# Kernel tuning notes

Measured on AMD Instinct MI355X. Metric: run time of the kernel, lower is better.

Reference implementation:

```python
import jax, jax.numpy as jnp
import numpy as np

N_NODES = 100000
N_EDGES = 1600000
D_FEAT = 64
UNITS = [128, 128]


def setup_inputs() -> dict:
    key = jax.random.key(0)
    ks = jax.random.split(key, 8)
    row = jax.random.randint(ks[0], (N_EDGES,), 0, N_NODES, dtype=jnp.int32)
    col = jax.random.randint(ks[1], (N_EDGES,), 0, N_NODES, dtype=jnp.int32)
    vals = jax.random.uniform(ks[2], (N_EDGES,), dtype=jnp.float32)
    H = jax.random.normal(ks[3], (N_NODES, D_FEAT), dtype=jnp.float32)
    W1 = jax.random.normal(ks[4], (D_FEAT, UNITS[0]), dtype=jnp.float32) * (1.0 / np.sqrt(D_FEAT))
    b1 = jnp.zeros((UNITS[0],), dtype=jnp.float32)
    W2 = jax.random.normal(ks[5], (UNITS[0], UNITS[1]), dtype=jnp.float32) * (1.0 / np.sqrt(UNITS[0]))
    b2 = jnp.zeros((UNITS[1],), dtype=jnp.float32)
    return {"row": row, "col": col, "vals": vals, "H": H,
            "W1": W1, "b1": b1, "W2": W2, "b2": b2}


def _spmm(row, col, vals, H, n_nodes):
    # sparse A (COO) @ dense H: gather source rows, scale, scatter-add to dest
    return jax.ops.segment_sum(vals[:, None] * H[col], row, num_segments=n_nodes)


def reference(row, col, vals, H, W1, b1, W2, b2):
    n = H.shape[0]
    # layer 0: AH @ W1 + b1, relu (source bug: relu applied since i < num_units-1)
    AH = _spmm(row, col, vals, H, n)
    H1 = jax.nn.relu(AH @ W1 + b1)
    # layer 1: same structure, also relu per source's activation condition
    AH1 = _spmm(row, col, vals, H1, n)
    H2 = jax.nn.relu(AH1 @ W2 + b2)
    return H2
```

## Files before the change

### kernel.cpp

```cpp
#include <hip/hip_runtime.h>


#define NFEAT 64
#define NHID 128
#define BSHIFT 9
#define BROWS (1 << BSHIFT)
#define NB_MAX 256

typedef __attribute__((ext_vector_type(8))) short bf16x8;
typedef __attribute__((ext_vector_type(4))) float f32x4;
typedef __attribute__((ext_vector_type(2))) float f32x2;

__device__ __forceinline__ unsigned short f2bf(float x) {
  unsigned u = __float_as_uint(x);
  unsigned r = (u + 0x7FFFu + ((u >> 16) & 1u)) >> 16;
  return (unsigned short)r;
}
__device__ __forceinline__ unsigned pack2(float a, float b) {
  return (unsigned)f2bf(a) | ((unsigned)f2bf(b) << 16);
}

__device__ __forceinline__ unsigned pk_fp8x4(float a, float b, float c, float d) {
  int w = __builtin_amdgcn_cvt_pk_fp8_f32(a, b, 0, false);
  w = __builtin_amdgcn_cvt_pk_fp8_f32(c, d, w, true);
  return (unsigned)w;
}
__device__ __forceinline__ unsigned char f2fp8(float x) {
  return (unsigned char)(__builtin_amdgcn_cvt_pk_fp8_f32(x, 0.f, 0, false) & 0xFF);
}

__device__ __forceinline__ void acc16(f32x2* a, uint4 q, float v) {
  f32x2 vv = {v, v};
  a[0] += vv * __builtin_amdgcn_cvt_pk_f32_fp8(q.x, false);
  a[1] += vv * __builtin_amdgcn_cvt_pk_f32_fp8(q.x, true);
  a[2] += vv * __builtin_amdgcn_cvt_pk_f32_fp8(q.y, false);
  a[3] += vv * __builtin_amdgcn_cvt_pk_f32_fp8(q.y, true);
  a[4] += vv * __builtin_amdgcn_cvt_pk_f32_fp8(q.z, false);
  a[5] += vv * __builtin_amdgcn_cvt_pk_f32_fp8(q.z, true);
  a[6] += vv * __builtin_amdgcn_cvt_pk_f32_fp8(q.w, false);
  a[7] += vv * __builtin_amdgcn_cvt_pk_f32_fp8(q.w, true);
}

template <int RS>
__device__ __forceinline__ void gather_row(
    const int2* __restrict__ sedge, const uint4* __restrict__ Hq,
    int beg, int end, int f, f32x2* a) {
  int j = beg;
  if ((j & 1) && j < end) {
    int2 ev = sedge[j];
    acc16(a, Hq[ev.x * RS + f], __int_as_float(ev.y));
    ++j;
  }
  if (j + 4 <= end) {
    const int4* mp = (const int4*)sedge;
    int4 m0 = mp[j >> 1], m1 = mp[(j >> 1) + 1];
    while (j + 8 <= end) {
      uint4 q0 = Hq[m0.x * RS + f];
      uint4 q1 = Hq[m0.z * RS + f];
      uint4 q2 = Hq[m1.x * RS + f];
      uint4 q3 = Hq[m1.z * RS + f];
      int4 n0 = mp[(j >> 1) + 2];
      int4 n1 = mp[(j >> 1) + 3];
      acc16(a, q0, __int_as_float(m0.y));
      acc16(a, q1, __int_as_float(m0.w));
      acc16(a, q2, __int_as_float(m1.y));
      acc16(a, q3, __int_as_float(m1.w));
      m0 = n0;
      m1 = n1;
      j += 4;
    }
    uint4 q0 = Hq[m0.x * RS + f];
    uint4 q1 = Hq[m0.z * RS + f];
    uint4 q2 = Hq[m1.x * RS + f];
    uint4 q3 = Hq[m1.z * RS + f];
    acc16(a, q0, __int_as_float(m0.y));
    acc16(a, q1, __int_as_float(m0.w));
    acc16(a, q2, __int_as_float(m1.y));
    acc16(a, q3, __int_as_float(m1.w));
    j += 4;
  }
  for (; j < end; ++j) {
    int2 ev = sedge[j];
    acc16(a, Hq[ev.x * RS + f], __int_as_float(ev.y));
  }
}

__global__ __launch_bounds__(256) void prep_kernel(
    const float* __restrict__ H, const float* __restrict__ W1,
    const float* __restrict__ W2, unsigned char* __restrict__ Hf8,
    unsigned short* __restrict__ Wsw1, unsigned short* __restrict__ Wsw2,
    int n8) {
  const int total = n8 + 64 * 128 + 128 * 128;
  for (int w = blockIdx.x * 256 + threadIdx.x; w < total; w += gridDim.x * 256) {
    if (w < n8) {
      float4 a = ((const float4*)H)[2 * w];
      float4 b = ((const float4*)H)[2 * w + 1];
      ((uint2*)Hf8)[w] = make_uint2(pk_fp8x4(a.x, a.y, a.z, a.w),
                                    pk_fp8x4(b.x, b.y, b.z, b.w));
    } else {
      int idx = w - n8;
      const float* W = W1;
      unsigned short* Wsw = Wsw1;
      if (idx >= 64 * 128) {
        idx -= 64 * 128;
        W = W2;
        Wsw = Wsw2;
      }
      int j = idx & 7, q = (idx >> 3) & 3, nn = (idx >> 5) & 127, kt = idx >> 12;
      int k = kt * 32 + q * 8 + j;
      Wsw[idx] = f2bf(W[(size_t)k * 128 + nn]);
    }
  }
}

__global__ __launch_bounds__(256) void bhist_kernel(
    const int* __restrict__ row, int* __restrict__ bcnt, int n_edges, int nb) {
  __shared__ int h[NB_MAX];
  for (int i = threadIdx.x; i < NB_MAX; i += 256) h[i] = 0;
  __syncthreads();
  const int n4 = n_edges >> 2;
  for (int i = blockIdx.x * 256 + threadIdx.x; i < n4; i += gridDim.x * 256) {
    int4 r4 = ((const int4*)row)[i];
    atomicAdd(&h[r4.x >> BSHIFT], 1);
    atomicAdd(&h[r4.y >> BSHIFT], 1);
    atomicAdd(&h[r4.z >> BSHIFT], 1);
    atomicAdd(&h[r4.w >> BSHIFT], 1);
  }
  if (blockIdx.x == 0 && threadIdx.x < (n_edges & 3))
    atomicAdd(&h[row[(n4 << 2) + threadIdx.x] >> BSHIFT], 1);
  __syncthreads();
  for (int i = threadIdx.x; i < nb; i += 256)
    if (h[i]) atomicAdd(&bcnt[i], h[i]);
}

__global__ __launch_bounds__(NB_MAX) void bscan_kernel(
    const int* __restrict__ bcnt, int* __restrict__ bbase, int* __restrict__ cur,
    int* __restrict__ row_ptr, int nb, int n) {
  __shared__ int sm[NB_MAX];
  int t = threadIdx.x;
  int v = (t < nb) ? bcnt[t] : 0;
  sm[t] = v;
  __syncthreads();
  for (int off = 1; off < NB_MAX; off <<= 1) {
    int u = (t >= off) ? sm[t - off] : 0;
    __syncthreads();
    sm[t] += u;
    __syncthreads();
  }
  if (t < nb) {
    bbase[t] = sm[t] - v;
    cur[t] = sm[t] - v;
  }
  if (t == nb - 1) {
    bbase[nb] = sm[t];
    row_ptr[n] = sm[t];
  }
}

__global__ __launch_bounds__(1024) void partition_kernel(
    const int* __restrict__ row, const int* __restrict__ col,
    const float* __restrict__ vals, int* __restrict__ cur,
    int2* __restrict__ bedge, int n_edges) {
  __shared__ int h[NB_MAX], base[NB_MAX], rk[NB_MAX];
  for (int i = threadIdx.x; i < NB_MAX; i += 1024) {
    h[i] = 0;
    rk[i] = 0;
  }
  __syncthreads();
  const int t0 = blockIdx.x * 1024 + threadIdx.x;
  const int T = gridDim.x * 1024;
  const int n4 = n_edges >> 2;
  for (int i = t0; i < n4; i += T) {
    int4 r4 = ((const int4*)row)[i];
    atomicAdd(&h[r4.x >> BSHIFT], 1);
    atomicAdd(&h[r4.y >> BSHIFT], 1);
    atomicAdd(&h[r4.z >> BSHIFT], 1);
    atomicAdd(&h[r4.w >> BSHIFT], 1);
  }
  if (blockIdx.x == 0 && threadIdx.x < (n_edges & 3))
    atomicAdd(&h[row[(n4 << 2) + threadIdx.x] >> BSHIFT], 1);
  __syncthreads();
  for (int i = threadIdx.x; i < NB_MAX; i += 1024)
    base[i] = h[i] ? atomicAdd(&cur[i], h[i]) : 0;
  __syncthreads();
  for (int i = t0; i < n4; i += T) {
    int4 r4 = ((const int4*)row)[i];
    int4 c4 = ((const int4*)col)[i];
    float4 v4 = ((const float4*)vals)[i];
    {
      int b = r4.x >> BSHIFT;
      int p = base[b] + atomicAdd(&rk[b], 1);
      bedge[p] = make_int2(((r4.x & (BROWS - 1)) << 17) | c4.x, __float_as_int(v4.x));
    }
    {
      int b = r4.y >> BSHIFT;
      int p = base[b] + atomicAdd(&rk[b], 1);
      bedge[p] = make_int2(((r4.y & (BROWS - 1)) << 17) | c4.y, __float_as_int(v4.y));
    }
    {
      int b = r4.z >> BSHIFT;
      int p = base[b] + atomicAdd(&rk[b], 1);
      bedge[p] = make_int2(((r4.z & (BROWS - 1)) << 17) | c4.z, __float_as_int(v4.z));
    }
    {
      int b = r4.w >> BSHIFT;
      int p = base[b] + atomicAdd(&rk[b], 1);
      bedge[p] = make_int2(((r4.w & (BROWS - 1)) << 17) | c4.w, __float_as_int(v4.w));
    }
  }
  if (blockIdx.x == 0 && threadIdx.x < (n_edges & 3)) {
    int e = (n4 << 2) + threadIdx.x;
    int r = row[e];
    int b = r >> BSHIFT;
    int p = base[b] + atomicAdd(&rk[b], 1);
    bedge[p] = make_int2(((r & (BROWS - 1)) << 17) | col[e], __float_as_int(vals[e]));
  }
}

__global__ __launch_bounds__(1024) void bucket_csr_kernel(
    const int* __restrict__ bbase, const int2* __restrict__ bedge,
    int* __restrict__ row_ptr, int2* __restrict__ sedge, int n) {
  __shared__ int cnt[BROWS];
  __shared__ int sm[BROWS];
  const int b = blockIdx.x;
  const int t = threadIdx.x;
  const int beg = bbase[b], end = bbase[b + 1];
  if (t < BROWS) cnt[t] = 0;
  __syncthreads();
  for (int j = beg + t; j < end; j += 1024)
    atomicAdd(&cnt[((unsigned)bedge[j].x) >> 17], 1);
  __syncthreads();
  int v = (t < BROWS) ? cnt[t] : 0;
  if (t < BROWS) sm[t] = v;
  __syncthreads();
  for (int off = 1; off < BROWS; off <<= 1) {
    int u = (t >= off && t < BROWS) ? sm[t - off] : 0;
    __syncthreads();
    if (t < BROWS) sm[t] += u;
    __syncthreads();
  }
  int incl = (t < BROWS) ? sm[t] : 0;
  __syncthreads();
  if (t < BROWS) {
    sm[t] = incl - v;
    int r = (b << BSHIFT) + t;
    if (r < n) row_ptr[r] = beg + sm[t];
    cnt[t] = 0;
  }
  __syncthreads();
  for (int j = beg + t; j < end; j += 1024) {
    int2 ev = bedge[j];
    int rl = ((unsigned)ev.x) >> 17;
    int rank = atomicAdd(&cnt[rl], 1);
    sedge[beg + sm[rl] + rank] = make_int2(ev.x & 0x1FFFF, ev.y);
  }
}

__global__ __launch_bounds__(128) void fused64_kernel(
    const int* __restrict__ row_ptr, const int2* __restrict__ sedge,
    const unsigned char* __restrict__ Hf8,
    const unsigned short* __restrict__ Wsw,
    const float* __restrict__ b, unsigned char* __restrict__ H1f8, int n) {
  __shared__ uint4 tile[32 * 9];
  const int tid = threadIdx.x;
  {
    const int rl = tid >> 2, f = tid & 3;
    const int r = blockIdx.x * 32 + rl;
    int beg = 0, end = 0;
    if (r < n) {
      beg = row_ptr[r];
      end = row_ptr[r + 1];
    }
    f32x2 a[8];
#pragma unroll
    for (int i = 0; i < 8; ++i) a[i] = (f32x2){0.f, 0.f};
    gather_row<4>(sedge, (const uint4*)Hf8, beg, end, f, a);
    tile[rl * 9 + f * 2] =
        make_uint4(pack2(a[0].x, a[0].y), pack2(a[1].x, a[1].y),
                   pack2(a[2].x, a[2].y), pack2(a[3].x, a[3].y));
    tile[rl * 9 + f * 2 + 1] =
        make_uint4(pack2(a[4].x, a[4].y), pack2(a[5].x, a[5].y),
                   pack2(a[6].x, a[6].y), pack2(a[7].x, a[7].y));
  }
  const int lane = tid & 63, wave = tid >> 6;
  const int m = lane & 15, quad = lane >> 4;
  bf16x8 bfr[2][8];
#pragma unroll
  for (int kt = 0; kt < 2; ++kt)
#pragma unroll
    for (int c = 0; c < 8; ++c)
      bfr[kt][c] = *(const bf16x8*)(Wsw + ((size_t)(kt * 128 + c * 16 + m)) * 32 + quad * 8);
  __syncthreads();
  f32x4 acc[8];
#pragma unroll
  for (int c = 0; c < 8; ++c) acc[c] = (f32x4){0.f, 0.f, 0.f, 0.f};
#pragma unroll
  for (int kt = 0; kt < 2; ++kt) {
    bf16x8 a = *(const bf16x8*)&tile[(wave * 16 + m) * 9 + kt * 4 + quad];
#pragma unroll
    for (int c = 0; c < 8; ++c)
      acc[c] = __builtin_amdgcn_mfma_f32_16x16x32_bf16(a, bfr[kt][c], acc[c], 0, 0, 0);
  }
  const int r0 = blockIdx.x * 32 + wave * 16;
#pragma unroll
  for (int c = 0; c < 8; ++c) {
    float bias = b[c * 16 + m];
#pragma unroll
    for (int i = 0; i < 4; ++i) {
      int rr = r0 + quad * 4 + i;
      if (rr >= n) continue;
      H1f8[(size_t)rr * 128 + c * 16 + m] = f2fp8(fmaxf(acc[c][i] + bias, 0.f));
    }
  }
}

__global__ __launch_bounds__(128) void fused128_kernel(
    const int* __restrict__ row_ptr, const int2* __restrict__ sedge,
    const unsigned char* __restrict__ H1f8,
    const unsigned short* __restrict__ Wsw,
    const float* __restrict__ b, float* __restrict__ out, int n) {
  __shared__ uint4 tile[16 * 17];
  const int tid = threadIdx.x;
  {
    const int rl = tid >> 3, f = tid & 7;
    const int r = blockIdx.x * 16 + rl;
    int beg = 0, end = 0;
    if (r < n) {
      beg = row_ptr[r];
      end = row_ptr[r + 1];
    }
    f32x2 a[8];
#pragma unroll
    for (int i = 0; i < 8; ++i) a[i] = (f32x2){0.f, 0.f};
    gather_row<8>(sedge, (const uint4*)H1f8, beg, end, f, a);
    tile[rl * 17 + f * 2] =
        make_uint4(pack2(a[0].x, a[0].y), pack2(a[1].x, a[1].y),
                   pack2(a[2].x, a[2].y), pack2(a[3].x, a[3].y));
    tile[rl * 17 + f * 2 + 1] =
        make_uint4(pack2(a[4].x, a[4].y), pack2(a[5].x, a[5].y),
                   pack2(a[6].x, a[6].y), pack2(a[7].x, a[7].y));
  }
  const int lane = tid & 63, wave = tid >> 6;
  const int m = lane & 15, quad = lane >> 4;
  const int h = wave;
  bf16x8 bfr[4][4];
#pragma unroll
  for (int kt = 0; kt < 4; ++kt)
#pragma unroll
    for (int c = 0; c < 4; ++c)
      bfr[kt][c] = *(const bf16x8*)(Wsw + ((size_t)(kt * 128 + (h * 4 + c) * 16 + m)) * 32 + quad * 8);
  __syncthreads();
  f32x4 acc[4];
#pragma unroll
  for (int c = 0; c < 4; ++c) acc[c] = (f32x4){0.f, 0.f, 0.f, 0.f};
#pragma unroll
  for (int kt = 0; kt < 4; ++kt) {
    bf16x8 a = *(const bf16x8*)&tile[m * 17 + kt * 4 + quad];
#pragma unroll
    for (int c = 0; c < 4; ++c)
      acc[c] = __builtin_amdgcn_mfma_f32_16x16x32_bf16(a, bfr[kt][c], acc[c], 0, 0, 0);
  }
  const int r0 = blockIdx.x * 16;
#pragma unroll
  for (int c = 0; c < 4; ++c) {
    float bias = b[(h * 4 + c) * 16 + m];
#pragma unroll
    for (int i = 0; i < 4; ++i) {
      int rr = r0 + quad * 4 + i;
      if (rr >= n) continue;
      out[(size_t)rr * 128 + (h * 4 + c) * 16 + m] = fmaxf(acc[c][i] + bias, 0.f);
    }
  }
}

__global__ __launch_bounds__(256) void spmm64_atomic(
    const int* __restrict__ row, const int* __restrict__ col,
    const float* __restrict__ vals, const float* __restrict__ Hin,
    float* __restrict__ out, int n_edges) {
  int tid = blockIdx.x * 256 + threadIdx.x;
  int e = tid >> 4, f = tid & 15;
  if (e >= n_edges) return;
  int c = col[e], r = row[e];
  float v = vals[e];
  float4 h = ((const float4*)Hin)[(size_t)c * 16 + f];
  float* o = out + (size_t)r * 64 + f * 4;
  atomicAdd(o + 0, v * h.x);
  atomicAdd(o + 1, v * h.y);
  atomicAdd(o + 2, v * h.z);
  atomicAdd(o + 3, v * h.w);
}

__global__ __launch_bounds__(256) void spmm128_atomic(
    const int* __restrict__ row, const int* __restrict__ col,
    const float* __restrict__ vals, const float* __restrict__ Hin,
    float* __restrict__ out, int n_edges) {
  int tid = blockIdx.x * 256 + threadIdx.x;
  int e = tid >> 5, f = tid & 31;
  if (e >= n_edges) return;
  int c = col[e], r = row[e];
  float v = vals[e];
  float4 h = ((const float4*)Hin)[(size_t)c * 32 + f];
  float* o = out + (size_t)r * 128 + f * 4;
  atomicAdd(o + 0, v * h.x);
  atomicAdd(o + 1, v * h.y);
  atomicAdd(o + 2, v * h.z);
  atomicAdd(o + 3, v * h.w);
}

template <int K>
__global__ __launch_bounds__(256) void gemm_tiled_relu(
    const float* __restrict__ A, const float* __restrict__ W,
    const float* __restrict__ b, float* __restrict__ out, int n) {
  constexpr int KB = 32;
  constexpr int RP = 132;
  __shared__ float As[KB][RP];
  __shared__ float Ws[KB][128];
  const int t = threadIdx.x;
  const int tx = t & 15, ty = t >> 4;
  const int r0 = blockIdx.x * 128;
  float4 acc0[8], acc1[8];
#pragma unroll
  for (int i = 0; i < 8; ++i) {
    acc0[i] = make_float4(0.f, 0.f, 0.f, 0.f);
    acc1[i] = make_float4(0.f, 0.f, 0.f, 0.f);
  }
  for (int k0 = 0; k0 < K; k0 += KB) {
#pragma unroll
    for (int q = 0; q < 4; ++q) {
      int f = q * 256 + t;
      int kk = f >> 5, cv = f & 31;
      ((float4*)&Ws[kk][0])[cv] = ((const float4*)(W + (size_t)(k0 + kk) * 128))[cv];
    }
#pragma unroll
    for (int q = 0; q < 4; ++q) {
      int f = q * 256 + t;
      int r = f >> 3, kv = f & 7;
      float4 av = make_float4(0.f, 0.f, 0.f, 0.f);
      if (r0 + r < n) av = ((const float4*)(A + (size_t)(r0 + r) * K + k0))[kv];
      As[4 * kv + 0][r] = av.x;
      As[4 * kv + 1][r] = av.y;
      As[4 * kv + 2][r] = av.z;
      As[4 * kv + 3][r] = av.w;
    }
    __syncthreads();
#pragma unroll
    for (int k = 0; k < KB; ++k) {
      float4 w0 = *((const float4*)&Ws[k][4 * tx]);
      float4 w1 = *((const float4*)&Ws[k][64 + 4 * tx]);
#pragma unroll
      for (int i = 0; i < 8; ++i) {
        float a = As[k][ty + 16 * i];
        acc0[i].x = fmaf(a, w0.x, acc0[i].x);
        acc0[i].y = fmaf(a, w0.y, acc0[i].y);
        acc0[i].z = fmaf(a, w0.z, acc0[i].z);
        acc0[i].w = fmaf(a, w0.w, acc0[i].w);
        acc1[i].x = fmaf(a, w1.x, acc1[i].x);
        acc1[i].y = fmaf(a, w1.y, acc1[i].y);
        acc1[i].z = fmaf(a, w1.z, acc1[i].z);
        acc1[i].w = fmaf(a, w1.w, acc1[i].w);
      }
    }
    __syncthreads();
  }
  float4 bb0 = ((const float4*)b)[tx];
  float4 bb1 = ((const float4*)(b + 64))[tx];
#pragma unroll
  for (int i = 0; i < 8; ++i) {
    int r = r0 + ty + 16 * i;
    if (r >= n) continue;
    float4 o0, o1;
    o0.x = fmaxf(acc0[i].x + bb0.x, 0.f);
    o0.y = fmaxf(acc0[i].y + bb0.y, 0.f);
    o0.z = fmaxf(acc0[i].z + bb0.z, 0.f);
    o0.w = fmaxf(acc0[i].w + bb0.w, 0.f);
    o1.x = fmaxf(acc1[i].x + bb1.x, 0.f);
    o1.y = fmaxf(acc1[i].y + bb1.y, 0.f);
    o1.z = fmaxf(acc1[i].z + bb1.z, 0.f);
    o1.w = fmaxf(acc1[i].w + bb1.w, 0.f);
    ((float4*)(out + (size_t)r * 128))[tx] = o0;
    ((float4*)(out + (size_t)r * 128 + 64))[tx] = o1;
  }
}

extern "C" void kernel_launch(void* const* d_in, const int* in_sizes, int n_in,
                              void* d_out, int out_size, void* d_ws, size_t ws_size,
                              hipStream_t stream) {
  const int* row = (const int*)d_in[0];
  const int* col = (const int*)d_in[1];
  const float* vals = (const float*)d_in[2];
  const float* H = (const float*)d_in[3];
  const float* W1 = (const float*)d_in[4];
  const float* b1 = (const float*)d_in[5];
  const float* W2 = (const float*)d_in[6];
  const float* b2 = (const float*)d_in[7];
  float* out = (float*)d_out;

  const int n_edges = in_sizes[0];
  const int n_nodes = in_sizes[3] / NFEAT;
  const int nb = (n_nodes + BROWS - 1) / BROWS;

  size_t off = 0;
  char* base = (char*)d_ws;
  int2* bedge = (int2*)(base + off);  off += (size_t)n_edges * 8;
  unsigned char* Hf8 = (unsigned char*)(base + off);   off += (size_t)n_nodes * NFEAT;
  unsigned char* H1f8 = (unsigned char*)(base + off);  off += (size_t)n_nodes * NHID;
  int2* sedge = (int2*)(base + off);  off += (size_t)n_edges * 8;
  unsigned short* Wsw1 = (unsigned short*)(base + off); off += 64 * 128 * 2;
  unsigned short* Wsw2 = (unsigned short*)(base + off); off += 128 * 128 * 2;
  int* bcnt = (int*)(base + off);     off += NB_MAX * 4;
  int* bbase = (int*)(base + off);    off += (NB_MAX + 1) * 4;
  int* cur = (int*)(base + off);      off += NB_MAX * 4;
  int* row_ptr = (int*)(base + off);  off += ((size_t)n_nodes + 1) * 4;
  const size_t needed = off;

  if (ws_size >= needed && nb <= NB_MAX && n_nodes <= (1 << 17)) {
    hipMemsetAsync(bcnt, 0, NB_MAX * sizeof(int), stream);
    bhist_kernel<<<1024, 256, 0, stream>>>(row, bcnt, n_edges, nb);
    bscan_kernel<<<1, NB_MAX, 0, stream>>>(bcnt, bbase, cur, row_ptr, nb, n_nodes);
    partition_kernel<<<256, 1024, 0, stream>>>(row, col, vals, cur, bedge, n_edges);
    bucket_csr_kernel<<<nb, 1024, 0, stream>>>(bbase, bedge, row_ptr, sedge, n_nodes);

    prep_kernel<<<1024, 256, 0, stream>>>(H, W1, W2, Hf8, Wsw1, Wsw2,
                                          n_nodes * NFEAT / 8);

    fused64_kernel<<<(n_nodes + 31) / 32, 128, 0, stream>>>(
        row_ptr, sedge, Hf8, Wsw1, b1, H1f8, n_nodes);
    fused128_kernel<<<(n_nodes + 15) / 16, 128, 0, stream>>>(
        row_ptr, sedge, H1f8, Wsw2, b2, out, n_nodes);
  } else {
    float* fAH = (float*)d_ws;
    float* fH1 = fAH + (size_t)n_nodes * NFEAT;
    hipMemsetAsync(fAH, 0, (size_t)n_nodes * NFEAT * sizeof(float), stream);
    hipMemsetAsync(out, 0, (size_t)n_nodes * NHID * sizeof(float), stream);
    spmm64_atomic<<<(n_edges * 16 + 255) / 256, 256, 0, stream>>>(row, col, vals, H, fAH, n_edges);
    gemm_tiled_relu<64><<<(n_nodes + 127) / 128, 256, 0, stream>>>(fAH, W1, b1, fH1, n_nodes);
    spmm128_atomic<<<(n_edges * 32 + 255) / 256, 256, 0, stream>>>(row, col, vals, fH1, out, n_edges);
    gemm_tiled_relu<128><<<(n_nodes + 127) / 128, 256, 0, stream>>>(out, W2, b2, out, n_nodes);
  }
}
```

Baseline: 261.5 us.

## Split layer-2 fused gather+GEMM into separate SpMM and MFMA GEMM kernels

Replaces the fused layer-2 kernel, which gathered neighbour rows into shared memory and then ran MFMA on them, with two kernels. The first does the CSR SpMM over the FP8 H1 and writes a bf16 intermediate into workspace that reuses the bucketed-edge slab. The second is a standalone MFMA GEMM that applies bias and ReLU. The aim is to let the gather run at full occupancy, free of the shared-memory tile and barrier, while the GEMM loads its weights once per 64 rows. The cost is an extra global write and read of a 100k x 128 bf16 intermediate and one more kernel launch.

```diff
diff --git a/kernel.cpp b/kernel.cpp
--- a/kernel.cpp
+++ b/kernel.cpp
@@ -314,61 +314,67 @@
   }
 }
 
-__global__ __launch_bounds__(128) void fused128_kernel(
+__global__ __launch_bounds__(256) void spmm128_csr_f8(
     const int* __restrict__ row_ptr, const int2* __restrict__ sedge,
-    const unsigned char* __restrict__ H1f8,
+    const unsigned char* __restrict__ Hf8, unsigned short* __restrict__ outbf,
+    int n) {
+  int tid = blockIdx.x * 256 + threadIdx.x;
+  int r = tid >> 3;
+  int f = tid & 7;
+  if (r >= n) return;
+  int beg = row_ptr[r], end = row_ptr[r + 1];
+  f32x2 a[8];
+#pragma unroll
+  for (int i = 0; i < 8; ++i) a[i] = (f32x2){0.f, 0.f};
+  gather_row<8>(sedge, (const uint4*)Hf8, beg, end, f, a);
+  uint4 o0 = make_uint4(pack2(a[0].x, a[0].y), pack2(a[1].x, a[1].y),
+                        pack2(a[2].x, a[2].y), pack2(a[3].x, a[3].y));
+  uint4 o1 = make_uint4(pack2(a[4].x, a[4].y), pack2(a[5].x, a[5].y),
+                        pack2(a[6].x, a[6].y), pack2(a[7].x, a[7].y));
+  ((uint4*)outbf)[(size_t)r * 16 + f * 2] = o0;
+  ((uint4*)outbf)[(size_t)r * 16 + f * 2 + 1] = o1;
+}
+
+__global__ __launch_bounds__(256) void gemm128_mfma_relu(
+    const unsigned short* __restrict__ Abf,
     const unsigned short* __restrict__ Wsw,
     const float* __restrict__ b, float* __restrict__ out, int n) {
-  __shared__ uint4 tile[16 * 17];
-  const int tid = threadIdx.x;
-  {
-    const int rl = tid >> 3, f = tid & 7;
-    const int r = blockIdx.x * 16 + rl;
-    int beg = 0, end = 0;
-    if (r < n) {
-      beg = row_ptr[r];
-      end = row_ptr[r + 1];
-    }
-    f32x2 a[8];
-#pragma unroll
-    for (int i = 0; i < 8; ++i) a[i] = (f32x2){0.f, 0.f};
-    gather_row<8>(sedge, (const uint4*)H1f8, beg, end, f, a);
-    tile[rl * 17 + f * 2] =
-        make_uint4(pack2(a[0].x, a[0].y), pack2(a[1].x, a[1].y),
-                   pack2(a[2].x, a[2].y), pack2(a[3].x, a[3].y));
-    tile[rl * 17 + f * 2 + 1] =
-        make_uint4(pack2(a[4].x, a[4].y), pack2(a[5].x, a[5].y),
-                   pack2(a[6].x, a[6].y), pack2(a[7].x, a[7].y));
-  }
-  const int lane = tid & 63, wave = tid >> 6;
-  const int m = lane & 15, quad = lane >> 4;
-  const int h = wave;
-  bf16x8 bfr[4][4];
+  const int lane = threadIdx.x & 63;
+  const int wave = threadIdx.x >> 6;
+  const int m = lane & 15;
+  const int quad = lane >> 4;
+  const int r0 = blockIdx.x * 64 + wave * 16;
+
+  bf16x8 bfr[4][8];
 #pragma unroll
   for (int kt = 0; kt < 4; ++kt)
 #pragma unroll
-    for (int c = 0; c < 4; ++c)
-      bfr[kt][c] = *(const bf16x8*)(Wsw + ((size_t)(kt * 128 + (h * 4 + c) * 16 + m)) * 32 + quad * 8);
-  __syncthreads();
-  f32x4 acc[4];
-#pragma unroll
-  for (int c = 0; c < 4; ++c) acc[c] = (f32x4){0.f, 0.f, 0.f, 0.f};
+    for (int c = 0; c < 8; ++c)
+      bfr[kt][c] = *(const bf16x8*)(Wsw + ((size_t)(kt * 128 + c * 16 + m)) * 32 + quad * 8);
+
+  f32x4 acc[8];
+#pragma unroll
+  for (int c = 0; c < 8; ++c) acc[c] = (f32x4){0.f, 0.f, 0.f, 0.f};
+
+  int row = r0 + m;
+  if (row >= n) row = n - 1;
+  const uint4* Arow = (const uint4*)(Abf + (size_t)row * 128);
 #pragma unroll
   for (int kt = 0; kt < 4; ++kt) {
-    bf16x8 a = *(const bf16x8*)&tile[m * 17 + kt * 4 + quad];
-#pragma unroll
-    for (int c = 0; c < 4; ++c)
+    bf16x8 a = *(const bf16x8*)&Arow[kt * 4 + quad];
+#pragma unroll
+    for (int c = 0; c < 8; ++c)
       acc[c] = __builtin_amdgcn_mfma_f32_16x16x32_bf16(a, bfr[kt][c], acc[c], 0, 0, 0);
   }
-  const int r0 = blockIdx.x * 16;
-#pragma unroll
-  for (int c = 0; c < 4; ++c) {
-    float bias = b[(h * 4 + c) * 16 + m];
+
+#pragma unroll
+  for (int c = 0; c < 8; ++c) {
+    float bias = b[c * 16 + m];
 #pragma unroll
     for (int i = 0; i < 4; ++i) {
       int rr = r0 + quad * 4 + i;
       if (rr >= n) continue;
-      out[(size_t)rr * 128 + (h * 4 + c) * 16 + m] = fmaxf(acc[c][i] + bias, 0.f);
+      out[(size_t)rr * 128 + c * 16 + m] = fmaxf(acc[c][i] + bias, 0.f);
     }
   }
 }
@@ -501,7 +507,11 @@
 
   size_t off = 0;
   char* base = (char*)d_ws;
-  int2* bedge = (int2*)(base + off);  off += (size_t)n_edges * 8;
+  char* slab0 = base;
+  size_t slab0_sz = (size_t)n_edges * 8;
+  size_t ah1_sz = (size_t)n_nodes * NHID * 2;
+  if (ah1_sz > slab0_sz) slab0_sz = ah1_sz;
+  off += slab0_sz;
   unsigned char* Hf8 = (unsigned char*)(base + off);   off += (size_t)n_nodes * NFEAT;
   unsigned char* H1f8 = (unsigned char*)(base + off);  off += (size_t)n_nodes * NHID;
   int2* sedge = (int2*)(base + off);  off += (size_t)n_edges * 8;
@@ -512,6 +522,8 @@
   int* cur = (int*)(base + off);      off += NB_MAX * 4;
   int* row_ptr = (int*)(base + off);  off += ((size_t)n_nodes + 1) * 4;
   const size_t needed = off;
+  int2* bedge = (int2*)slab0;
+  unsigned short* AH1bf = (unsigned short*)slab0;
 
   if (ws_size >= needed && nb <= NB_MAX && n_nodes <= (1 << 17)) {
     hipMemsetAsync(bcnt, 0, NB_MAX * sizeof(int), stream);
@@ -525,8 +537,10 @@
 
     fused64_kernel<<<(n_nodes + 31) / 32, 128, 0, stream>>>(
         row_ptr, sedge, Hf8, Wsw1, b1, H1f8, n_nodes);
-    fused128_kernel<<<(n_nodes + 15) / 16, 128, 0, stream>>>(
-        row_ptr, sedge, H1f8, Wsw2, b2, out, n_nodes);
+    spmm128_csr_f8<<<(n_nodes * 8 + 255) / 256, 256, 0, stream>>>(
+        row_ptr, sedge, H1f8, AH1bf, n_nodes);
+    gemm128_mfma_relu<<<(n_nodes + 63) / 64, 256, 0, stream>>>(
+        AH1bf, Wsw2, b2, out, n_nodes);
   } else {
     float* fAH = (float*)d_ws;
     float* fH1 = fAH + (size_t)n_nodes * NFEAT;
```

Result: slower. 268.9 us (+2.8%).
